# Performance work log

Hardware: AMD Instinct MI355X
Metric: run time of the kernel (lower is better)

Reference implementation:

```python
import jax, jax.numpy as jnp
import numpy as np

B, T, C = 4, 2048, 768
H, D = 12, 64          # num heads, head size
MLP = 3072
EPS = 1e-6
SCALE = C ** (-0.5)    # NOTE: source scales by n_embd**-0.5, not head_size**-0.5


def setup_inputs() -> dict:
    key = jax.random.key(0)
    ks = jax.random.split(key, 12)
    s = 0.02
    return {
        "x":     jax.random.normal(ks[0], (B, T, C), jnp.float32),
        "Wq":    jax.random.normal(ks[1], (H, C, D), jnp.float32) * s,
        "Wk":    jax.random.normal(ks[2], (H, C, D), jnp.float32) * s,
        "Wv":    jax.random.normal(ks[3], (H, C, D), jnp.float32) * s,
        "Wo":    jax.random.normal(ks[4], (H * D, C), jnp.float32) * s,
        "bo":    jnp.zeros((C,), jnp.float32),
        "ln1_g": jnp.ones((C,), jnp.float32),
        "ln1_b": jnp.zeros((C,), jnp.float32),
        "ln2_g": jnp.ones((C,), jnp.float32),
        "ln2_b": jnp.zeros((C,), jnp.float32),
        "W1":    jax.random.normal(ks[5], (C, MLP), jnp.float32) * s,
        "b1":    jnp.zeros((MLP,), jnp.float32),
        "W2":    jax.random.normal(ks[6], (MLP, C), jnp.float32) * s,
        "b2":    jnp.zeros((C,), jnp.float32),
    }


def _ln(x, g, b):
    mu = jnp.mean(x, axis=-1, keepdims=True)
    var = jnp.var(x, axis=-1, keepdims=True)
    return (x - mu) * jax.lax.rsqrt(var + EPS) * g + b


def reference(x, Wq, Wk, Wv, Wo, bo, ln1_g, ln1_b, ln2_g, ln2_b, W1, b1, W2, b2):
    xn = _ln(x, ln1_g, ln1_b)
    # batched per-head projections: [B,T,C] x [H,C,D] -> [B,H,T,D]
    q = jnp.einsum("btc,hcd->bhtd", xn, Wq)
    k = jnp.einsum("btc,hcd->bhtd", xn, Wk)
    v = jnp.einsum("btc,hcd->bhtd", xn, Wv)
    wei = jnp.einsum("bhtd,bhsd->bhts", q, k) * SCALE  # [B,H,T,T]
    wei = jax.nn.softmax(wei, axis=-1)
    attn = jnp.einsum("bhts,bhsd->bhtd", wei, v)
    # concat heads along feature dim (head order preserved)
    attn = attn.transpose(0, 2, 1, 3).reshape(B, T, H * D)
    sa = attn @ Wo + bo
    x2 = sa + x                      # residual 1 (dropout = identity in eval)
    y = _ln(x2, ln2_g, ln2_b)
    y = jax.nn.gelu(y @ W1 + b1, approximate=False) @ W2 + b2
    return x2 + y                    # residual 2
```

## Files before the change

kernel.cpp:

```cpp
#include <hip/hip_runtime.h>
#include <hip/hip_bf16.h>
#include <cstdint>
#include <cmath>

#define B_ 4
#define T_ 2048
#define C_ 768
#define H_ 12
#define D_ 64
#define MLP_ 3072
#define BT_ (B_*T_)

typedef __hip_bfloat16 hbf;
typedef __bf16 bf16_t;
typedef bf16_t bf16x8 __attribute__((ext_vector_type(8)));
typedef bf16_t bf16x4 __attribute__((ext_vector_type(4)));
typedef float f32x4 __attribute__((ext_vector_type(4)));

static __device__ __forceinline__ void load_lds16(const void* g, void* l) {
    __builtin_amdgcn_global_load_lds(
        (const __attribute__((address_space(1))) unsigned int*)g,
        (__attribute__((address_space(3))) unsigned int*)l, 16, 0, 0);
}

__global__ __launch_bounds__(256) void transpose_pack(
    const float* __restrict__ src, hbf* __restrict__ dst, int R, int S)
{
    __shared__ float tl[64 * 65];
    src += (size_t)blockIdx.z * R * S;
    dst += (size_t)blockIdx.z * R * S;
    const int r0 = blockIdx.y * 64, s0 = blockIdx.x * 64;
    const int c = threadIdx.x & 63, q = threadIdx.x >> 6;
#pragma unroll
    for (int j = 0; j < 16; ++j) {
        int r = q + j * 4;
        tl[r * 65 + c] = src[(size_t)(r0 + r) * S + s0 + c];
    }
    __syncthreads();
#pragma unroll
    for (int j = 0; j < 16; ++j) {
        int s = q + j * 4;
        dst[(size_t)(s0 + s) * R + r0 + c] = __float2bfloat16(tl[c * 65 + s]);
    }
}

__global__ __launch_bounds__(256) void pack_qkv3(
    const float* __restrict__ Wq, const float* __restrict__ Wk,
    const float* __restrict__ Wv, hbf* __restrict__ WqkT, hbf* __restrict__ WvT)
{
    __shared__ float tl[64 * 65];
    const int z = blockIdx.z;
    const int mtx = z / 12, head = z - mtx * 12;
    const float* src = (mtx == 0 ? Wq : mtx == 1 ? Wk : Wv) + (size_t)head * 49152;
    hbf* dst = (mtx == 2) ? (WvT + (size_t)head * 49152)
                          : (WqkT + (size_t)(mtx * 12 + head) * 49152);
    const int r0 = blockIdx.y * 64;
    const int c = threadIdx.x & 63, q = threadIdx.x >> 6;
#pragma unroll
    for (int j = 0; j < 16; ++j) {
        int r = q + j * 4;
        tl[r * 65 + c] = src[(size_t)(r0 + r) * 64 + c];
    }
    __syncthreads();
#pragma unroll
    for (int j = 0; j < 16; ++j) {
        int s = q + j * 4;
        dst[(size_t)s * 768 + r0 + c] = __float2bfloat16(tl[c * 65 + s]);
    }
}

__global__ __launch_bounds__(256) void ln_kernel(
    const float* __restrict__ x, const float* __restrict__ g,
    const float* __restrict__ bb, hbf* __restrict__ out)
{
    __shared__ float red[8];
    const int row = blockIdx.x;
    const float* xr = x + (size_t)row * C_;
    const int t = threadIdx.x;
    float v0 = xr[t], v1 = xr[t + 256], v2 = xr[t + 512];
    float s = v0 + v1 + v2;
    float s2 = v0 * v0 + v1 * v1 + v2 * v2;
#pragma unroll
    for (int m = 1; m < 64; m <<= 1) {
        s  += __shfl_xor(s,  m, 64);
        s2 += __shfl_xor(s2, m, 64);
    }
    if ((t & 63) == 0) { red[t >> 6] = s; red[4 + (t >> 6)] = s2; }
    __syncthreads();
    float S  = red[0] + red[1] + red[2] + red[3];
    float S2 = red[4] + red[5] + red[6] + red[7];
    float mu  = S * (1.0f / C_);
    float var = S2 * (1.0f / C_) - mu * mu;
    float inv = rsqrtf(var + 1e-6f);
    hbf* orow = out + (size_t)row * C_;
    orow[t]       = __float2bfloat16((v0 - mu) * inv * g[t]       + bb[t]);
    orow[t + 256] = __float2bfloat16((v1 - mu) * inv * g[t + 256] + bb[t + 256]);
    orow[t + 512] = __float2bfloat16((v2 - mu) * inv * g[t + 512] + bb[t + 512]);
}

template<int EPI, int TN>
__global__ __launch_bounds__(256, 3) void gemm_kernel(
    const hbf* __restrict__ A, const hbf* __restrict__ Bt,
    float* __restrict__ outF, hbf* __restrict__ outH,
    const float* __restrict__ bias, const float* __restrict__ resid,
    int M, int N, int K,
    hbf* __restrict__ qb, hbf* __restrict__ kb,
    float scale, int gx)
{
    constexpr int AM = (TN == 128) ? 4 : 2;
    constexpr int NB_B = (TN == 128) ? 4 : 2;
    __shared__ hbf sA[128 * 64];
    __shared__ hbf sB[TN * 64];
    const int tid = threadIdx.x;
    const int lane = tid & 63;
    const int wid = tid >> 6;
    const int lr = lane & 15, hg = lane >> 4;
    const int bid = blockIdx.x, nwg = gridDim.x;
    const int wg = (bid & 7) * (nwg >> 3) + (bid >> 3);
    const int bx = wg % gx, by = wg / gx;
    const int row0 = by * 128;
    const int col0 = bx * TN;
    const int wrow = (TN == 128) ? (wid >> 1) * 64 : wid * 32;
    const int wcol = (TN == 128) ? (wid & 1) * 64 : 0;

    f32x4 acc[AM][4] = {};

    int offG[4];
    const int Kb = K * 2;
#pragma unroll
    for (int i = 0; i < 4; ++i) {
        int c = tid + i * 256;
        offG[i] = (c >> 3) * Kb + (((c & 7) ^ ((c >> 3) & 7)) << 4);
    }
    const char* gA = (const char*)(A + (size_t)row0 * K);
    const char* gB = (const char*)(Bt + (size_t)col0 * K);

    auto stage = [&](int kt) {
        const int kb2 = kt * 128;
#pragma unroll
        for (int i = 0; i < 4; ++i)
            load_lds16(gA + (size_t)(offG[i] + kb2), (char*)sA + i * 4096 + wid * 1024);
#pragma unroll
        for (int i = 0; i < NB_B; ++i)
            load_lds16(gB + (size_t)(offG[i] + kb2), (char*)sB + i * 4096 + wid * 1024);
    };

    const int NK = K >> 6;
    stage(0);
    for (int kt = 0; kt < NK; ++kt) {
        __syncthreads();
#pragma unroll
        for (int kf = 0; kf < 2; ++kf) {
            const int sl = ((kf * 4 + hg) ^ (lr & 7)) << 4;
            bf16x8 af[AM], bfr[4];
#pragma unroll
            for (int m = 0; m < AM; ++m)
                af[m] = *(const bf16x8*)((const char*)sA + (wrow + m * 16 + lr) * 128 + sl);
#pragma unroll
            for (int n = 0; n < 4; ++n)
                bfr[n] = *(const bf16x8*)((const char*)sB + (wcol + n * 16 + lr) * 128 + sl);
#pragma unroll
            for (int m = 0; m < AM; ++m)
#pragma unroll
                for (int n = 0; n < 4; ++n)
                    acc[m][n] = __builtin_amdgcn_mfma_f32_16x16x32_bf16(af[m], bfr[n], acc[m][n], 0, 0, 0);
        }
        __syncthreads();
        if (kt + 1 < NK) stage(kt + 1);
    }

#pragma unroll
    for (int m = 0; m < AM; ++m) {
#pragma unroll
        for (int n = 0; n < 4; ++n) {
#pragma unroll
            for (int j = 0; j < 4; ++j) {
                int row = row0 + wrow + m * 16 + hg * 4 + j;
                int col = col0 + wcol + n * 16 + lr;
                float v = acc[m][n][j];
                if constexpr (EPI == 0) {
                    outH[(size_t)row * N + col] = __float2bfloat16(v);
                } else if constexpr (EPI == 1) {
                    outF[(size_t)row * N + col] = v + bias[col] + resid[(size_t)row * N + col];
                } else if constexpr (EPI == 2) {
                    float tt = v + bias[col];
                    float ge = 0.5f * tt * (1.0f + erff(tt * 0.70710678118654752f));
                    outH[(size_t)row * N + col] = __float2bfloat16(ge);
                } else {
                    int typ = col / C_;
                    int rr = col - typ * C_;
                    int h = rr >> 6, d = rr & 63;
                    int b = row >> 11, t = row & (T_ - 1);
                    size_t bh = (size_t)b * H_ + h;
                    if (typ == 0) qb[(bh * T_ + t) * D_ + d] = __float2bfloat16(v * scale);
                    else          kb[(bh * T_ + t) * D_ + d] = __float2bfloat16(v);
                }
            }
        }
    }
}

__global__ __launch_bounds__(256, 3) void attn_kernel(
    const hbf* __restrict__ qg, const hbf* __restrict__ kg,
    const hbf* __restrict__ vg, hbf* __restrict__ outA)
{
    __shared__ hbf sK0[64 * 64], sK1[64 * 64];
    __shared__ hbf sV0[64 * 64], sV1[64 * 64];
    __shared__ hbf sP[4 * 32 * 64];
    const int tid = threadIdx.x, lane = tid & 63, wid = tid >> 6;
    const int lr = lane & 15, hg = lane >> 4;
    const int wg = (blockIdx.x & 7) * 96 + (blockIdx.x >> 3);
    const int bh = wg >> 4;
    const int b = bh / H_, h = bh - b * H_;
    const int wr0 = (wg & 15) * 128 + wid * 32;
    const hbf* qbh = qg + (size_t)bh * T_ * D_;
    const hbf* kbh = kg + (size_t)bh * T_ * D_;
    const hbf* vbh = vg + (size_t)h * 64 * BT_ + (size_t)b * T_;

    bf16x8 a_q[2][2];
#pragma unroll
    for (int m = 0; m < 2; ++m)
#pragma unroll
        for (int kf = 0; kf < 2; ++kf)
            a_q[m][kf] = *(const bf16x8*)(qbh + (size_t)(wr0 + m * 16 + lr) * D_ + kf * 32 + hg * 8);

    f32x4 o[2][4] = {};
    float mreg[2] = {-3e38f, -3e38f};
    float lrun[2] = {0.0f, 0.0f};

    int offK[2], offV[2];
#pragma unroll
    for (int i = 0; i < 2; ++i) {
        int c = tid + i * 256;
        int sw = ((c & 7) ^ ((c >> 3) & 7)) << 4;
        offK[i] = (c >> 3) * 128 + sw;
        offV[i] = (c >> 3) * (BT_ * 2) + sw;
    }
    hbf* sPw = sP + wid * (32 * 64);
    const int sl0 = ((0 * 4 + hg) ^ (lr & 7)) << 4;
    const int sl1 = ((1 * 4 + hg) ^ (lr & 7)) << 4;
    const int bcast = hg * 20;

    auto stage = [&](int itn, hbf* sKd, hbf* sVd) {
        const char* kp = (const char*)kbh + (size_t)itn * 8192;
        const char* vp = (const char*)vbh + (size_t)itn * 128;
#pragma unroll
        for (int i = 0; i < 2; ++i) {
            load_lds16(kp + offK[i], (char*)sKd + i * 4096 + wid * 1024);
            load_lds16(vp + offV[i], (char*)sVd + i * 4096 + wid * 1024);
        }
    };

    auto tile = [&](const hbf* sKc, const hbf* sVc) {
        f32x4 st[4][2] = {};
        __builtin_amdgcn_s_setprio(1);
#pragma unroll
        for (int kf = 0; kf < 2; ++kf) {
            const int sl = kf ? sl1 : sl0;
#pragma unroll
            for (int n = 0; n < 4; ++n) {
                bf16x8 ak = *(const bf16x8*)((const char*)sKc + (n * 16 + lr) * 128 + sl);
                st[n][0] = __builtin_amdgcn_mfma_f32_16x16x32_bf16(ak, a_q[0][kf], st[n][0], 0, 0, 0);
                st[n][1] = __builtin_amdgcn_mfma_f32_16x16x32_bf16(ak, a_q[1][kf], st[n][1], 0, 0, 0);
            }
        }
        __builtin_amdgcn_s_setprio(0);

#pragma unroll
        for (int m = 0; m < 2; ++m) {
            float t = st[0][m][0];
#pragma unroll
            for (int n = 0; n < 4; ++n)
#pragma unroll
                for (int j = 0; j < 4; ++j)
                    if (n + j > 0) t = fmaxf(t, st[n][m][j]);
            t = fmaxf(t, __shfl_xor(t, 16, 64));
            t = fmaxf(t, __shfl_xor(t, 32, 64));
            if (__any(t - mreg[m] > 8.0f)) {
                float nm = fmaxf(mreg[m], t);
                float fac = __expf(mreg[m] - nm);
                mreg[m] = nm;
                lrun[m] *= fac;
                float fb[4];
#pragma unroll
                for (int j = 0; j < 4; ++j)
                    fb[j] = __shfl(fac, bcast + j, 64);
#pragma unroll
                for (int nd = 0; nd < 4; ++nd)
#pragma unroll
                    for (int j = 0; j < 4; ++j)
                        o[m][nd][j] *= fb[j];
            }
            float ps = 0.0f;
            const int r = m * 16 + lr;
#pragma unroll
            for (int n = 0; n < 4; ++n) {
                float p0 = __expf(st[n][m][0] - mreg[m]);
                float p1 = __expf(st[n][m][1] - mreg[m]);
                float p2 = __expf(st[n][m][2] - mreg[m]);
                float p3 = __expf(st[n][m][3] - mreg[m]);
                ps += (p0 + p1) + (p2 + p3);
                bf16x4 w;
                w[0] = (bf16_t)p0; w[1] = (bf16_t)p1; w[2] = (bf16_t)p2; w[3] = (bf16_t)p3;
                *(bf16x4*)((char*)sPw + r * 128 +
                           (((n * 2 + (hg >> 1)) ^ (r & 7)) << 4) + ((hg & 1) * 8)) = w;
            }
            ps += __shfl_xor(ps, 16, 64);
            ps += __shfl_xor(ps, 32, 64);
            lrun[m] += ps;
        }

        __builtin_amdgcn_s_setprio(1);
#pragma unroll
        for (int kf = 0; kf < 2; ++kf) {
            const int sl = kf ? sl1 : sl0;
            bf16x8 ap0 = *(const bf16x8*)((const char*)sPw + lr * 128 + sl);
            bf16x8 ap1 = *(const bf16x8*)((const char*)sPw + (16 + lr) * 128 + sl);
#pragma unroll
            for (int nd = 0; nd < 4; ++nd) {
                bf16x8 bv = *(const bf16x8*)((const char*)sVc + (nd * 16 + lr) * 128 + sl);
                o[0][nd] = __builtin_amdgcn_mfma_f32_16x16x32_bf16(ap0, bv, o[0][nd], 0, 0, 0);
                o[1][nd] = __builtin_amdgcn_mfma_f32_16x16x32_bf16(ap1, bv, o[1][nd], 0, 0, 0);
            }
        }
        __builtin_amdgcn_s_setprio(0);
    };

    const int NT = T_ / 64;
    stage(0, sK0, sV0);
    __syncthreads();
    for (int it = 0; it < NT; it += 2) {
        stage(it + 1, sK1, sV1);
        tile(sK0, sV0);
        __syncthreads();
        if (it + 2 < NT) stage(it + 2, sK0, sV0);
        tile(sK1, sV1);
        __syncthreads();
    }

    float lb[2][4];
#pragma unroll
    for (int m = 0; m < 2; ++m)
#pragma unroll
        for (int j = 0; j < 4; ++j)
            lb[m][j] = __shfl(lrun[m], bcast + j, 64);
#pragma unroll
    for (int m = 0; m < 2; ++m)
#pragma unroll
        for (int nd = 0; nd < 4; ++nd)
#pragma unroll
            for (int j = 0; j < 4; ++j) {
                int row = wr0 + m * 16 + hg * 4 + j;
                int col = nd * 16 + lr;
                float val = o[m][nd][j] / lb[m][j];
                outA[((size_t)(b * T_ + row)) * C_ + h * D_ + col] = __float2bfloat16(val);
            }
}

extern "C" void kernel_launch(void* const* d_in, const int* in_sizes, int n_in,
                              void* d_out, int out_size, void* d_ws, size_t ws_size,
                              hipStream_t stream)
{
    const float* x    = (const float*)d_in[0];
    const float* Wq   = (const float*)d_in[1];
    const float* Wk   = (const float*)d_in[2];
    const float* Wv   = (const float*)d_in[3];
    const float* Wo   = (const float*)d_in[4];
    const float* bo   = (const float*)d_in[5];
    const float* ln1g = (const float*)d_in[6];
    const float* ln1b = (const float*)d_in[7];
    const float* ln2g = (const float*)d_in[8];
    const float* ln2b = (const float*)d_in[9];
    const float* W1   = (const float*)d_in[10];
    const float* b1   = (const float*)d_in[11];
    const float* W2   = (const float*)d_in[12];
    const float* b2   = (const float*)d_in[13];
    float* out = (float*)d_out;
    char* ws = (char*)d_ws;

    hbf*  xn    = (hbf*)(ws + 0);
    hbf*  WqkT  = (hbf*)(ws + 12582912);
    hbf*  WvT   = (hbf*)(ws + 14942208);
    hbf*  qb    = (hbf*)(ws + 16121856);
    hbf*  kb    = (hbf*)(ws + 28704768);
    hbf*  vT    = (hbf*)(ws + 41287680);
    hbf*  h1    = (hbf*)(ws + 0);
    hbf*  attnB = (hbf*)(ws + 53870592);
    hbf*  yln   = (hbf*)(ws + 53870592);
    float* x2   = (float*)(ws + 66453504);
    hbf*  WoT   = (hbf*)(ws + 91619328);
    hbf*  W1T   = (hbf*)(ws + 92798976);
    hbf*  W2T   = (hbf*)(ws + 97517568);

    const float SCALE = 0.036084391824351615f;

    pack_qkv3<<<dim3(1, 12, 36), 256, 0, stream>>>(Wq, Wk, Wv, WqkT, WvT);
    transpose_pack<<<dim3(12, 12, 1), 256, 0, stream>>>(Wo, WoT, 768, 768);
    transpose_pack<<<dim3(48, 12, 1), 256, 0, stream>>>(W1, W1T, 768, 3072);
    transpose_pack<<<dim3(12, 48, 1), 256, 0, stream>>>(W2, W2T, 3072, 768);
    ln_kernel<<<8192, 256, 0, stream>>>(x, ln1g, ln1b, xn);
    gemm_kernel<3,128><<<768, 256, 0, stream>>>(xn, WqkT, nullptr, nullptr, nullptr, nullptr,
        8192, 1536, 768, qb, kb, SCALE, 12);
    gemm_kernel<0,128><<<384, 256, 0, stream>>>(WvT, xn, nullptr, vT, nullptr, nullptr,
        768, BT_, 768, nullptr, nullptr, 1.0f, 64);
    attn_kernel<<<768, 256, 0, stream>>>(qb, kb, vT, attnB);
    gemm_kernel<1,64><<<768, 256, 0, stream>>>(attnB, WoT, x2, nullptr, bo, x,
        8192, 768, 768, nullptr, nullptr, 1.0f, 12);
    ln_kernel<<<8192, 256, 0, stream>>>(x2, ln2g, ln2b, yln);
    gemm_kernel<2,128><<<1536, 256, 0, stream>>>(yln, W1T, nullptr, h1, b1, nullptr,
        8192, 3072, 768, nullptr, nullptr, 1.0f, 24);
    gemm_kernel<1,64><<<768, 256, 0, stream>>>(h1, W2T, out, nullptr, b2, x2,
        8192, 768, 3072, nullptr, nullptr, 1.0f, 12);
}
```

Before: 289.5 us.

## Fuse V projection into QKV GEMM, store residual in bf16, raise TN=64 occupancy

The V projection is folded into the Q/K GEMM by packing Wv alongside Wq/Wk (N=2304) and writing V transposed in the epilogue with vectorized bf16x4 stores, removing a separate GEMM launch and a second read of xn. The intermediate residual x2 is now kept in bf16 rather than fp32, halving its write and its two reads (LN2 and final GEMM), at some cost in precision of the residual path. Launch bounds for the TN=64 GEMMs are raised to 4 blocks per CU, which may squeeze registers.

```diff
diff --git a/kernel.cpp b/kernel.cpp
--- a/kernel.cpp
+++ b/kernel.cpp
@@ -46,14 +46,13 @@
 
 __global__ __launch_bounds__(256) void pack_qkv3(
     const float* __restrict__ Wq, const float* __restrict__ Wk,
-    const float* __restrict__ Wv, hbf* __restrict__ WqkT, hbf* __restrict__ WvT)
+    const float* __restrict__ Wv, hbf* __restrict__ WqkT)
 {
     __shared__ float tl[64 * 65];
     const int z = blockIdx.z;
     const int mtx = z / 12, head = z - mtx * 12;
     const float* src = (mtx == 0 ? Wq : mtx == 1 ? Wk : Wv) + (size_t)head * 49152;
-    hbf* dst = (mtx == 2) ? (WvT + (size_t)head * 49152)
-                          : (WqkT + (size_t)(mtx * 12 + head) * 49152);
+    hbf* dst = WqkT + (size_t)z * 49152;
     const int r0 = blockIdx.y * 64;
     const int c = threadIdx.x & 63, q = threadIdx.x >> 6;
 #pragma unroll
@@ -69,15 +68,23 @@
     }
 }
 
+template<typename TI>
 __global__ __launch_bounds__(256) void ln_kernel(
-    const float* __restrict__ x, const float* __restrict__ g,
+    const TI* __restrict__ x, const float* __restrict__ g,
     const float* __restrict__ bb, hbf* __restrict__ out)
 {
     __shared__ float red[8];
     const int row = blockIdx.x;
-    const float* xr = x + (size_t)row * C_;
+    const TI* xr = x + (size_t)row * C_;
     const int t = threadIdx.x;
-    float v0 = xr[t], v1 = xr[t + 256], v2 = xr[t + 512];
+    float v0, v1, v2;
+    if constexpr (__is_same(TI, float)) {
+        v0 = xr[t]; v1 = xr[t + 256]; v2 = xr[t + 512];
+    } else {
+        v0 = __bfloat162float(xr[t]);
+        v1 = __bfloat162float(xr[t + 256]);
+        v2 = __bfloat162float(xr[t + 512]);
+    }
     float s = v0 + v1 + v2;
     float s2 = v0 * v0 + v1 * v1 + v2 * v2;
 #pragma unroll
@@ -99,12 +106,13 @@
 }
 
 template<int EPI, int TN>
-__global__ __launch_bounds__(256, 3) void gemm_kernel(
+__global__ __launch_bounds__(256, (TN == 64) ? 4 : 3) void gemm_kernel(
     const hbf* __restrict__ A, const hbf* __restrict__ Bt,
     float* __restrict__ outF, hbf* __restrict__ outH,
-    const float* __restrict__ bias, const float* __restrict__ resid,
+    const float* __restrict__ bias, const float* __restrict__ residF,
+    const hbf* __restrict__ residH,
     int M, int N, int K,
-    hbf* __restrict__ qb, hbf* __restrict__ kb,
+    hbf* __restrict__ qb, hbf* __restrict__ kb, hbf* __restrict__ vt,
     float scale, int gx)
 {
     constexpr int AM = (TN == 128) ? 4 : 2;
@@ -173,20 +181,29 @@
     for (int m = 0; m < AM; ++m) {
 #pragma unroll
         for (int n = 0; n < 4; ++n) {
+            const int colc = col0 + wcol + n * 16 + lr;
+            const int rowb = row0 + wrow + m * 16 + hg * 4;
+            if constexpr (EPI == 3) {
+                if (colc >= 2 * C_) {
+                    bf16x4 w;
+#pragma unroll
+                    for (int j = 0; j < 4; ++j) w[j] = (bf16_t)acc[m][n][j];
+                    *(bf16x4*)(vt + (size_t)(colc - 2 * C_) * BT_ + rowb) = w;
+                    continue;
+                }
+            }
 #pragma unroll
             for (int j = 0; j < 4; ++j) {
-                int row = row0 + wrow + m * 16 + hg * 4 + j;
-                int col = col0 + wcol + n * 16 + lr;
+                int row = rowb + j;
+                int col = colc;
                 float v = acc[m][n][j];
                 if constexpr (EPI == 0) {
                     outH[(size_t)row * N + col] = __float2bfloat16(v);
-                } else if constexpr (EPI == 1) {
-                    outF[(size_t)row * N + col] = v + bias[col] + resid[(size_t)row * N + col];
                 } else if constexpr (EPI == 2) {
                     float tt = v + bias[col];
                     float ge = 0.5f * tt * (1.0f + erff(tt * 0.70710678118654752f));
                     outH[(size_t)row * N + col] = __float2bfloat16(ge);
-                } else {
+                } else if constexpr (EPI == 3) {
                     int typ = col / C_;
                     int rr = col - typ * C_;
                     int h = rr >> 6, d = rr & 63;
@@ -194,6 +211,12 @@
                     size_t bh = (size_t)b * H_ + h;
                     if (typ == 0) qb[(bh * T_ + t) * D_ + d] = __float2bfloat16(v * scale);
                     else          kb[(bh * T_ + t) * D_ + d] = __float2bfloat16(v);
+                } else if constexpr (EPI == 4) {
+                    outH[(size_t)row * N + col] =
+                        __float2bfloat16(v + bias[col] + residF[(size_t)row * N + col]);
+                } else {
+                    outF[(size_t)row * N + col] =
+                        v + bias[col] + __bfloat162float(residH[(size_t)row * N + col]);
                 }
             }
         }
@@ -380,35 +403,32 @@
 
     hbf*  xn    = (hbf*)(ws + 0);
     hbf*  WqkT  = (hbf*)(ws + 12582912);
-    hbf*  WvT   = (hbf*)(ws + 14942208);
     hbf*  qb    = (hbf*)(ws + 16121856);
     hbf*  kb    = (hbf*)(ws + 28704768);
     hbf*  vT    = (hbf*)(ws + 41287680);
     hbf*  h1    = (hbf*)(ws + 0);
     hbf*  attnB = (hbf*)(ws + 53870592);
     hbf*  yln   = (hbf*)(ws + 53870592);
-    float* x2   = (float*)(ws + 66453504);
+    hbf*  x2b   = (hbf*)(ws + 66453504);
     hbf*  WoT   = (hbf*)(ws + 91619328);
     hbf*  W1T   = (hbf*)(ws + 92798976);
     hbf*  W2T   = (hbf*)(ws + 97517568);
 
     const float SCALE = 0.036084391824351615f;
 
-    pack_qkv3<<<dim3(1, 12, 36), 256, 0, stream>>>(Wq, Wk, Wv, WqkT, WvT);
+    pack_qkv3<<<dim3(1, 12, 36), 256, 0, stream>>>(Wq, Wk, Wv, WqkT);
     transpose_pack<<<dim3(12, 12, 1), 256, 0, stream>>>(Wo, WoT, 768, 768);
     transpose_pack<<<dim3(48, 12, 1), 256, 0, stream>>>(W1, W1T, 768, 3072);
     transpose_pack<<<dim3(12, 48, 1), 256, 0, stream>>>(W2, W2T, 3072, 768);
-    ln_kernel<<<8192, 256, 0, stream>>>(x, ln1g, ln1b, xn);
-    gemm_kernel<3,128><<<768, 256, 0, stream>>>(xn, WqkT, nullptr, nullptr, nullptr, nullptr,
-        8192, 1536, 768, qb, kb, SCALE, 12);
-    gemm_kernel<0,128><<<384, 256, 0, stream>>>(WvT, xn, nullptr, vT, nullptr, nullptr,
-        768, BT_, 768, nullptr, nullptr, 1.0f, 64);
+    ln_kernel<float><<<8192, 256, 0, stream>>>(x, ln1g, ln1b, xn);
+    gemm_kernel<3,128><<<1152, 256, 0, stream>>>(xn, WqkT, nullptr, nullptr, nullptr, nullptr,
+        nullptr, 8192, 2304, 768, qb, kb, vT, SCALE, 18);
     attn_kernel<<<768, 256, 0, stream>>>(qb, kb, vT, attnB);
-    gemm_kernel<1,64><<<768, 256, 0, stream>>>(attnB, WoT, x2, nullptr, bo, x,
-        8192, 768, 768, nullptr, nullptr, 1.0f, 12);
-    ln_kernel<<<8192, 256, 0, stream>>>(x2, ln2g, ln2b, yln);
+    gemm_kernel<4,64><<<768, 256, 0, stream>>>(attnB, WoT, nullptr, x2b, bo, x,
+        nullptr, 8192, 768, 768, nullptr, nullptr, nullptr, 1.0f, 12);
+    ln_kernel<hbf><<<8192, 256, 0, stream>>>(x2b, ln2g, ln2b, yln);
     gemm_kernel<2,128><<<1536, 256, 0, stream>>>(yln, W1T, nullptr, h1, b1, nullptr,
-        8192, 3072, 768, nullptr, nullptr, 1.0f, 24);
-    gemm_kernel<1,64><<<768, 256, 0, stream>>>(h1, W2T, out, nullptr, b2, x2,
-        8192, 768, 3072, nullptr, nullptr, 1.0f, 12);
-}
+        nullptr, 8192, 3072, 768, nullptr, nullptr, nullptr, 1.0f, 24);
+    gemm_kernel<5,64><<<768, 256, 0, stream>>>(h1, W2T, out, nullptr, b2, nullptr,
+        x2b, 8192, 768, 3072, nullptr, nullptr, nullptr, 1.0f, 12);
+}
```

New measurement: 283.6 us. 2.0% less time.
